# Performance work log

Measured on AMD Instinct MI355X. Metric: run time of the kernel, lower is better.

The kernel has to match this reference:

```python
import jax, jax.numpy as jnp
import numpy as np

B, N, D = 4, 4096, 512
E, H, TOPK = 4, 2048, 1
V_MAX, FEAT_CLAMP = 3.0, 10.0


def setup_inputs() -> dict:
    key = jax.random.key(0)
    ks = jax.random.split(key, 8)
    g = lambda k, shape, s: (jax.random.normal(k, shape, jnp.float32) * s)
    return {
        "x": g(ks[0], (B, N, D), 1.0),
        "gate_w": g(ks[1], (D, E), 0.02), "gate_b": jnp.zeros((E,), jnp.float32),
        "w1": g(ks[2], (E, D, H), 0.02), "b1": jnp.zeros((E, H), jnp.float32),
        "w2": g(ks[3], (E, H, D), 0.02), "b2": jnp.zeros((E, D), jnp.float32),
        "v_w": g(ks[4], (D,), 0.02), "v_b": jnp.zeros((), jnp.float32),
        "out_w": g(ks[5], (2, D), 0.02), "out_b": jnp.zeros((D,), jnp.float32),
        "bk_scale": jnp.asarray(1.0, jnp.float32),
    }


def _moe_ffn(x, gate_w, gate_b, w1, b1, w2, b2):
    # Sparse MoE FFN (eval mode, no dropout): top-k routing, softmax over top-k logits.
    logits = x @ gate_w + gate_b                       # (B,N,E)
    vals, idx = jax.lax.top_k(logits, TOPK)            # (B,N,K)
    wts = jax.nn.softmax(vals, axis=-1)                # (B,N,K); == 1.0 for top_k=1
    wfull = jnp.sum(jax.nn.one_hot(idx, E, dtype=x.dtype) * wts[..., None], axis=-2)  # (B,N,E)
    h = jax.nn.gelu(jnp.einsum('bnd,edh->benh', x, w1) + b1[None, :, None, :])
    y = jnp.einsum('benh,ehd->bend', h, w2) + b2[None, :, None, :]
    return jnp.einsum('bne,bend->bnd', wfull, y)


def _tridiag_green_diag(diag, sup, sub, z):
    # Diagonal of G = (T - z I)^{-1} for tridiagonal T via stable continuant ratios:
    #   L_i = theta_i/theta_{i-1},  R_i = phi_i/phi_{i+1},  G_ii = 1/(L_i + R_i - d_i)
    d = diag.astype(jnp.complex64) - z                 # (B,N)
    s = (sub * sup).astype(jnp.complex64)              # (B,N-1)
    dT = jnp.swapaxes(d, 0, 1)                         # (N,B)
    sT = jnp.swapaxes(s, 0, 1)                         # (N-1,B)

    def step(carry, inp):
        di, si = inp
        nxt = di - si / carry
        return nxt, nxt

    _, Lrest = jax.lax.scan(step, dT[0], (dT[1:], sT))
    L = jnp.concatenate([dT[:1], Lrest], axis=0)       # (N,B)
    _, Rrest = jax.lax.scan(step, dT[-1], (dT[:-1][::-1], sT[::-1]))
    R = jnp.concatenate([dT[-1:], Rrest], axis=0)[::-1]
    G = 1.0 / (L + R - dT)                             # (N,B)
    return jnp.swapaxes(G, 0, 1)                       # (B,N)


def reference(x, gate_w, gate_b, w1, b1, w2, b2, v_w, v_b, out_w, out_b, bk_scale):
    ffn_out = _moe_ffn(x, gate_w, gate_b, w1, b1, w2, b2)        # (B,N,D)
    v = jnp.clip(ffn_out @ v_w + v_b, -V_MAX, V_MAX)             # (B,N)
    he_diag = v - 2.0                                            # h0_diag_base = -2
    ones_off = jnp.ones((x.shape[0], x.shape[1] - 1), x.dtype)   # h0 sub/super = 1
    G = _tridiag_green_diag(he_diag, ones_off, ones_off, jnp.complex64(1j))
    feats = jnp.clip(jnp.stack([G.real, G.imag], axis=-1), -FEAT_CLAMP, FEAT_CLAMP)  # (B,N,2)
    spec = feats @ out_w + out_b                                 # (B,N,D)
    return ffn_out + bk_scale * spec
```

## Files before the change

kernel.cpp:

```cpp
#include <hip/hip_runtime.h>
#include <hip/hip_bf16.h>
#include <stdint.h>

#define TOK 16384
#define NSEQ 4096
#define BATCH 4
#define Dm 512
#define Em 4
#define Hm 2048

typedef __attribute__((ext_vector_type(4))) float f32x4;
typedef __attribute__((ext_vector_type(4))) unsigned int u32x4;

__device__ __forceinline__ unsigned short f2bf(float f) {
    union { float f; uint32_t u; } v; v.f = f;
    uint32_t u = v.u;
    uint32_t r = (u + 0x7FFFu + ((u >> 16) & 1u)) >> 16;
    return (unsigned short)r;
}

struct cpx { float re, im; };
__device__ __forceinline__ cpx cmul(cpx a, cpx b) { return { a.re*b.re - a.im*b.im, a.re*b.im + a.im*b.re }; }
__device__ __forceinline__ cpx csub(cpx a, cpx b) { return { a.re - b.re, a.im - b.im }; }
__device__ __forceinline__ cpx cadd(cpx a, cpx b) { return { a.re + b.re, a.im + b.im }; }
__device__ __forceinline__ cpx cdiv(cpx a, cpx b) {
    float inv = 1.0f / (b.re*b.re + b.im*b.im);
    return { (a.re*b.re + a.im*b.im)*inv, (a.im*b.re - a.re*b.im)*inv };
}

__device__ __forceinline__ void mfma_bf16(f32x4& acc, u32x4 a, u32x4 b) {
    asm("v_mfma_f32_16x16x32_bf16 %0, %1, %2, %0" : "+v"(acc) : "v"(a), "v"(b));
}

#define GLOAD_LDS16(g, l) \
    __builtin_amdgcn_global_load_lds((const __attribute__((address_space(1))) unsigned int*)(g), \
                                     (__attribute__((address_space(3))) unsigned int*)(l), 16, 0, 0)

__global__ __launch_bounds__(256) void gate_kernel(
    const float* __restrict__ x, const float* __restrict__ gate_w, const float* __restrict__ gate_b,
    unsigned short* __restrict__ xbf, int* __restrict__ expert_id)
{
    int wid = threadIdx.x >> 6, lane = threadIdx.x & 63;
    int t0 = (blockIdx.x * 4 + wid) * 8;

    const float4* gw4 = (const float4*)gate_w;
    float4 g[8];
#pragma unroll
    for (int j = 0; j < 8; j++) g[j] = gw4[lane * 8 + j];
    double gb0 = (double)gate_b[0], gb1 = (double)gate_b[1];
    double gb2 = (double)gate_b[2], gb3 = (double)gate_b[3];

    for (int tt = 0; tt < 8; tt++) {
        int t = t0 + tt;
        const float4* x4 = (const float4*)(x + (size_t)t * Dm);
        float4 xa = x4[lane * 2], xb = x4[lane * 2 + 1];

        uint4 pk;
        pk.x = (uint32_t)f2bf(xa.x) | ((uint32_t)f2bf(xa.y) << 16);
        pk.y = (uint32_t)f2bf(xa.z) | ((uint32_t)f2bf(xa.w) << 16);
        pk.z = (uint32_t)f2bf(xb.x) | ((uint32_t)f2bf(xb.y) << 16);
        pk.w = (uint32_t)f2bf(xb.z) | ((uint32_t)f2bf(xb.w) << 16);
        *(uint4*)(xbf + (size_t)t * Dm + lane * 8) = pk;

        float xv[8] = { xa.x, xa.y, xa.z, xa.w, xb.x, xb.y, xb.z, xb.w };
        double s0 = 0, s1 = 0, s2 = 0, s3 = 0;
#pragma unroll
        for (int j = 0; j < 8; j++) {
            s0 += (double)xv[j] * (double)g[j].x;
            s1 += (double)xv[j] * (double)g[j].y;
            s2 += (double)xv[j] * (double)g[j].z;
            s3 += (double)xv[j] * (double)g[j].w;
        }
#pragma unroll
        for (int off = 1; off < 64; off <<= 1) {
            s0 += __shfl_xor(s0, off);
            s1 += __shfl_xor(s1, off);
            s2 += __shfl_xor(s2, off);
            s3 += __shfl_xor(s3, off);
        }
        if (lane == 0) {
            double l0 = s0 + gb0, l1 = s1 + gb1, l2 = s2 + gb2, l3 = s3 + gb3;
            int e = 0; double best = l0;
            if (l1 > best) { best = l1; e = 1; }
            if (l2 > best) { best = l2; e = 2; }
            if (l3 > best) { best = l3; e = 3; }
            expert_id[t] = e;
        }
    }
}

__global__ __launch_bounds__(256) void transpose_cvt(
    const float* __restrict__ w1, const float* __restrict__ w2,
    unsigned short* __restrict__ w1t, unsigned short* __restrict__ w2t)
{
    int z = blockIdx.z;
    const float* src; unsigned short* dst; int R, C;
    if (z < 4) { src = w1 + (size_t)z * Dm * Hm; dst = w1t + (size_t)z * Hm * Dm; R = Dm; C = Hm; }
    else       { src = w2 + (size_t)(z - 4) * Hm * Dm; dst = w2t + (size_t)(z - 4) * Dm * Hm; R = Hm; C = Dm; }
    int c0 = blockIdx.x * 32, r0 = blockIdx.y * 32;
    if (c0 >= C || r0 >= R) return;
    __shared__ float tile[32][33];
    int tx = threadIdx.x & 31, ty = threadIdx.x >> 5;
#pragma unroll
    for (int i = 0; i < 4; i++)
        tile[ty + i * 8][tx] = src[(size_t)(r0 + ty + i * 8) * C + c0 + tx];
    __syncthreads();
#pragma unroll
    for (int i = 0; i < 4; i++)
        dst[(size_t)(c0 + ty + i * 8) * R + r0 + tx] = f2bf(tile[tx][ty + i * 8]);
}

__global__ __launch_bounds__(1024) void route_kernel(
    const int* __restrict__ expert_id, int* __restrict__ counts,
    int* __restrict__ offsets, int* __restrict__ rowmap)
{
    __shared__ int wcnt[16][4];
    __shared__ int woff[16][4];
    int wid = threadIdx.x >> 6, lane = threadIdx.x & 63;
    int base = wid * 1024;

    int myeid[16], myrank[16];
    int run0 = 0, run1 = 0, run2 = 0, run3 = 0;
#pragma unroll
    for (int s = 0; s < 16; s++) {
        int e = expert_id[base + s * 64 + lane];
        myeid[s] = e;
        unsigned long long b0 = __ballot(e & 1);
        unsigned long long b1 = __ballot(e & 2);
        unsigned long long m0 = (e & 1) ? b0 : ~b0;
        unsigned long long m1 = (e & 2) ? b1 : ~b1;
        unsigned long long same = m0 & m1;
        unsigned long long below = same & ((1ull << lane) - 1ull);
        int runh = (e == 0) ? run0 : (e == 1) ? run1 : (e == 2) ? run2 : run3;
        myrank[s] = runh + (int)__popcll(below);
        run0 += (int)__popcll(~b0 & ~b1);
        run1 += (int)__popcll(b0 & ~b1);
        run2 += (int)__popcll(~b0 & b1);
        run3 += (int)__popcll(b0 & b1);
    }
    if (lane == 0) {
        wcnt[wid][0] = run0; wcnt[wid][1] = run1; wcnt[wid][2] = run2; wcnt[wid][3] = run3;
    }
    __syncthreads();
    if (threadIdx.x == 0) {
        int t0 = 0, t1 = 0, t2 = 0, t3 = 0;
        for (int w = 0; w < 16; w++) {
            woff[w][0] = t0; woff[w][1] = t1; woff[w][2] = t2; woff[w][3] = t3;
            t0 += wcnt[w][0]; t1 += wcnt[w][1]; t2 += wcnt[w][2]; t3 += wcnt[w][3];
        }
        counts[0] = t0; counts[1] = t1; counts[2] = t2; counts[3] = t3;
        int o0 = 0, o1 = t0, o2 = t0 + t1, o3 = t0 + t1 + t2;
        offsets[0] = o0; offsets[1] = o1; offsets[2] = o2; offsets[3] = o3;
        for (int w = 0; w < 16; w++) {
            woff[w][0] += o0; woff[w][1] += o1; woff[w][2] += o2; woff[w][3] += o3;
        }
    }
    __syncthreads();
#pragma unroll
    for (int s = 0; s < 16; s++) {
        int e = myeid[s];
        rowmap[woff[wid][e] + myrank[s]] = base + s * 64 + lane;
    }
}

template<int KTOT, int NTOT, bool GATHER_A, bool GELU_EPI>
__global__ __launch_bounds__(256) void gemm_kernel(
    const unsigned short* __restrict__ A, const unsigned short* __restrict__ B,
    const float* __restrict__ bias,
    const int* __restrict__ counts, const int* __restrict__ offsets,
    const int* __restrict__ rowmap,
    unsigned short* __restrict__ Hout, float* __restrict__ Cout)
{
    int e = blockIdx.z;
    int Me = counts[e];
    int mblk = blockIdx.y;
    if (mblk * 128 >= Me) return;
    int base = offsets[e];
    int nblk = blockIdx.x;
    int t = threadIdx.x, wid = t >> 6, lane = t & 63;

    __shared__ __align__(16) unsigned short As[128 * 64];
    __shared__ __align__(16) unsigned short Bs[128 * 64];

    const unsigned short* agp[4];
    const unsigned short* bgp[4];
#pragma unroll
    for (int c = 0; c < 4; c++) {
        int f = c * 256 + t;
        int r = f >> 3;
        int kb = (f & 7) ^ (r & 7);
        int mr = mblk * 128 + r; if (mr >= Me) mr = Me - 1;
        int arow = GATHER_A ? rowmap[base + mr] : (base + mr);
        agp[c] = A + (size_t)arow * KTOT + kb * 8;
        int nr = nblk * 128 + r;
        bgp[c] = B + ((size_t)e * NTOT + nr) * (size_t)KTOT + kb * 8;
    }

    f32x4 acc[4][4] = {};
    int wm = wid >> 1, wn = wid & 1;

    for (int kt = 0; kt < KTOT / 64; kt++) {
        __syncthreads();
#pragma unroll
        for (int c = 0; c < 4; c++) {
            GLOAD_LDS16(agp[c] + kt * 64, As + (size_t)(c * 256 + wid * 64) * 8);
            GLOAD_LDS16(bgp[c] + kt * 64, Bs + (size_t)(c * 256 + wid * 64) * 8);
        }
        __syncthreads();
#pragma unroll
        for (int ks = 0; ks < 2; ks++) {
            u32x4 av[4], bv[4];
#pragma unroll
            for (int m = 0; m < 4; m++) {
                int ra = wm * 64 + m * 16 + (lane & 15);
                int g = (ks * 4 + (lane >> 4)) ^ (ra & 7);
                av[m] = *(const u32x4*)((const char*)As + ra * 128 + g * 16);
            }
#pragma unroll
            for (int n = 0; n < 4; n++) {
                int rb = wn * 64 + n * 16 + (lane & 15);
                int g = (ks * 4 + (lane >> 4)) ^ (rb & 7);
                bv[n] = *(const u32x4*)((const char*)Bs + rb * 128 + g * 16);
            }
#pragma unroll
            for (int m = 0; m < 4; m++)
#pragma unroll
                for (int n = 0; n < 4; n++)
                    mfma_bf16(acc[m][n], av[m], bv[n]);
        }
    }

#pragma unroll
    for (int n = 0; n < 4; n++) {
        int col = nblk * 128 + wn * 64 + n * 16 + (lane & 15);
        float bv = bias[e * NTOT + col];
#pragma unroll
        for (int m = 0; m < 4; m++) {
            int rbase = wm * 64 + m * 16 + ((lane >> 4) << 2);
#pragma unroll
            for (int j = 0; j < 4; j++) {
                int row = mblk * 128 + rbase + j;
                if (row < Me) {
                    float v = acc[m][n][j] + bv;
                    if (GELU_EPI) {
                        float u = 0.7978845608f * (v + 0.044715f * v * v * v);
                        float ex = __expf(2.0f * u);
                        float th = 1.0f - 2.0f / (ex + 1.0f);
                        float hv = 0.5f * v * (1.0f + th);
                        Hout[(size_t)(base + row) * NTOT + col] = f2bf(hv);
                    } else {
                        int tok = rowmap[base + row];
                        Cout[(size_t)tok * Dm + col] = v;
                    }
                }
            }
        }
    }
}

__global__ __launch_bounds__(256) void vdot_kernel(
    const float* __restrict__ out, const float* __restrict__ v_w, const float* __restrict__ v_b,
    float* __restrict__ dre)
{
    int wid = threadIdx.x >> 6, lane = threadIdx.x & 63;
    int t = blockIdx.x * 4 + wid;
    const float4* o4 = (const float4*)(out + (size_t)t * Dm);
    const float4* w4 = (const float4*)v_w;
    float4 a = o4[lane * 2], b = o4[lane * 2 + 1];
    float4 wa = w4[lane * 2], wb = w4[lane * 2 + 1];
    float s = a.x*wa.x + a.y*wa.y + a.z*wa.z + a.w*wa.w
            + b.x*wb.x + b.y*wb.y + b.z*wb.z + b.w*wb.w;
#pragma unroll
    for (int off = 1; off < 64; off <<= 1) s += __shfl_xor(s, off);
    if (lane == 0) {
        float v = s + v_b[0];
        v = fminf(fmaxf(v, -3.0f), 3.0f);
        dre[t] = v - 2.0f;
    }
}

#define SDI(i) ((i) + ((i) >> 6))
__global__ __launch_bounds__(64) void scan_kernel(
    const float* __restrict__ dre, float2* __restrict__ Lf, float2* __restrict__ Rb)
{
    int b = blockIdx.x >> 1, dir = blockIdx.x & 1;
    int lane = threadIdx.x;
    __shared__ float sd[4096 + 64];
    const float* src = dre + b * NSEQ;
    for (int i = lane; i < NSEQ; i += 64)
        sd[SDI(i)] = src[dir ? (NSEQ - 1 - i) : i];
    __syncthreads();

    cpx m00 = {1, 0}, m01 = {0, 0}, m10 = {0, 0}, m11 = {1, 0};
    int s0i = lane * 64;
#pragma unroll 4
    for (int j = 0; j < 64; j++) {
        cpx d = { sd[SDI(s0i + j)], -1.0f };
        cpx n00 = csub(cmul(d, m00), m10);
        cpx n01 = csub(cmul(d, m01), m11);
        m10 = m00; m11 = m01; m00 = n00; m01 = n01;
        if ((j & 15) == 15) {
            float mx = fmaxf(fmaxf(fmaxf(fabsf(m00.re), fabsf(m00.im)), fmaxf(fabsf(m01.re), fabsf(m01.im))),
                             fmaxf(fmaxf(fabsf(m10.re), fabsf(m10.im)), fmaxf(fabsf(m11.re), fabsf(m11.im))));
            float r = 1.0f / mx;
            m00.re *= r; m00.im *= r; m01.re *= r; m01.im *= r;
            m10.re *= r; m10.im *= r; m11.re *= r; m11.im *= r;
        }
    }

#pragma unroll
    for (int off = 1; off < 64; off <<= 1) {
        cpx q00, q01, q10, q11;
        q00.re = __shfl_up(m00.re, off); q00.im = __shfl_up(m00.im, off);
        q01.re = __shfl_up(m01.re, off); q01.im = __shfl_up(m01.im, off);
        q10.re = __shfl_up(m10.re, off); q10.im = __shfl_up(m10.im, off);
        q11.re = __shfl_up(m11.re, off); q11.im = __shfl_up(m11.im, off);
        if (lane >= off) {
            cpx r00 = cadd(cmul(m00, q00), cmul(m01, q10));
            cpx r01 = cadd(cmul(m00, q01), cmul(m01, q11));
            cpx r10 = cadd(cmul(m10, q00), cmul(m11, q10));
            cpx r11 = cadd(cmul(m10, q01), cmul(m11, q11));
            m00 = r00; m01 = r01; m10 = r10; m11 = r11;
            float mx = fmaxf(fmaxf(fmaxf(fabsf(m00.re), fabsf(m00.im)), fmaxf(fabsf(m01.re), fabsf(m01.im))),
                             fmaxf(fmaxf(fabsf(m10.re), fabsf(m10.im)), fmaxf(fabsf(m11.re), fabsf(m11.im))));
            float r = 1.0f / mx;
            m00.re *= r; m00.im *= r; m01.re *= r; m01.im *= r;
            m10.re *= r; m10.im *= r; m11.re *= r; m11.im *= r;
        }
    }

    cpx e00, e10;
    e00.re = __shfl_up(m00.re, 1); e00.im = __shfl_up(m00.im, 1);
    e10.re = __shfl_up(m10.re, 1); e10.im = __shfl_up(m10.im, 1);
    if (lane == 0) { e00 = {1, 0}; e10 = {0, 0}; }

    float2* outp = dir ? Rb : Lf;
    cpx Linv = cdiv(e10, e00);
#pragma unroll 4
    for (int j = 0; j < 64; j++) {
        int p = s0i + j;
        cpx d = { sd[SDI(p)], -1.0f };
        cpx L = csub(d, Linv);
        int idx = dir ? (NSEQ - 1 - p) : p;
        outp[b * NSEQ + idx] = make_float2(L.re, L.im);
        float inv = 1.0f / (L.re * L.re + L.im * L.im);
        Linv.re = L.re * inv; Linv.im = -L.im * inv;
    }
}

__global__ __launch_bounds__(256) void final_kernel(
    float* __restrict__ out, const float* __restrict__ dre,
    const float2* __restrict__ Lf, const float2* __restrict__ Rb,
    const float* __restrict__ out_w, const float* __restrict__ out_b,
    const float* __restrict__ bk)
{
    int t = blockIdx.x * 2 + (threadIdx.x >> 7);
    int c = threadIdx.x & 127;
    float2 L = Lf[t], R = Rb[t];
    float dr = dre[t];
    float denr = L.x + R.x - dr;
    float deni = L.y + R.y + 1.0f;
    float inv = 1.0f / (denr * denr + deni * deni);
    float f0 = fminf(fmaxf(denr * inv, -10.0f), 10.0f);
    float f1 = fminf(fmaxf(-deni * inv, -10.0f), 10.0f);
    float bks = bk[0];
    const float4* ow0 = (const float4*)out_w;
    const float4* ow1 = (const float4*)(out_w + Dm);
    const float4* ob4 = (const float4*)out_b;
    float4* o4 = (float4*)(out + (size_t)t * Dm);
    float4 w0 = ow0[c], w1v = ow1[c], ob = ob4[c];
    float4 y = o4[c];
    y.x += bks * (f0 * w0.x + f1 * w1v.x + ob.x);
    y.y += bks * (f0 * w0.y + f1 * w1v.y + ob.y);
    y.z += bks * (f0 * w0.z + f1 * w1v.z + ob.z);
    y.w += bks * (f0 * w0.w + f1 * w1v.w + ob.w);
    o4[c] = y;
}

constexpr size_t OFF_XBF    = 0;
constexpr size_t OFF_W1T    = 16777216;
constexpr size_t OFF_W2T    = OFF_W1T + 8388608;
constexpr size_t OFF_H      = OFF_W2T + 8388608;
constexpr size_t OFF_ROWMAP = OFF_H + 67108864;
constexpr size_t OFF_EID    = OFF_ROWMAP + 65536;
constexpr size_t OFF_DRE    = OFF_EID + 65536;
constexpr size_t OFF_LF     = OFF_DRE + 65536;
constexpr size_t OFF_RB     = OFF_LF + 131072;
constexpr size_t OFF_CNT    = OFF_RB + 131072;

extern "C" void kernel_launch(void* const* d_in, const int* in_sizes, int n_in,
                              void* d_out, int out_size, void* d_ws, size_t ws_size,
                              hipStream_t stream)
{
    const float* x      = (const float*)d_in[0];
    const float* gate_w = (const float*)d_in[1];
    const float* gate_b = (const float*)d_in[2];
    const float* w1     = (const float*)d_in[3];
    const float* b1     = (const float*)d_in[4];
    const float* w2     = (const float*)d_in[5];
    const float* b2     = (const float*)d_in[6];
    const float* v_w    = (const float*)d_in[7];
    const float* v_b    = (const float*)d_in[8];
    const float* out_w  = (const float*)d_in[9];
    const float* out_b  = (const float*)d_in[10];
    const float* bk     = (const float*)d_in[11];
    float* out = (float*)d_out;
    char* ws = (char*)d_ws;

    unsigned short* xbf = (unsigned short*)(ws + OFF_XBF);
    unsigned short* w1t = (unsigned short*)(ws + OFF_W1T);
    unsigned short* w2t = (unsigned short*)(ws + OFF_W2T);
    unsigned short* hbf = (unsigned short*)(ws + OFF_H);
    int* rowmap  = (int*)(ws + OFF_ROWMAP);
    int* eid     = (int*)(ws + OFF_EID);
    float* dre   = (float*)(ws + OFF_DRE);
    float2* Lf   = (float2*)(ws + OFF_LF);
    float2* Rb   = (float2*)(ws + OFF_RB);
    int* counts  = (int*)(ws + OFF_CNT);
    int* offsets = counts + 4;

    (void)in_sizes; (void)n_in; (void)out_size; (void)ws_size;

    gate_kernel<<<TOK / 32, 256, 0, stream>>>(x, gate_w, gate_b, xbf, eid);
    transpose_cvt<<<dim3(64, 64, 8), 256, 0, stream>>>(w1, w2, w1t, w2t);
    route_kernel<<<1, 1024, 0, stream>>>(eid, counts, offsets, rowmap);

    gemm_kernel<512, 2048, true, true><<<dim3(16, 128, 4), 256, 0, stream>>>(
        xbf, w1t, b1, counts, offsets, rowmap, hbf, nullptr);
    gemm_kernel<2048, 512, false, false><<<dim3(4, 128, 4), 256, 0, stream>>>(
        hbf, w2t, b2, counts, offsets, rowmap, nullptr, out);

    vdot_kernel<<<TOK / 4, 256, 0, stream>>>(out, v_w, v_b, dre);
    scan_kernel<<<8, 64, 0, stream>>>(dre, Lf, Rb);
    final_kernel<<<TOK / 2, 256, 0, stream>>>(out, dre, Lf, Rb, out_w, out_b, bk);
}
```

Measured before the change: 221.8 us.

## Double-buffer LDS tiles in MoE GEMM to overlap global loads with MFMA

The expert GEMM kernel now uses two LDS buffers for its A and B tiles. The next k-tile is loaded with direct-to-LDS global loads while MFMAs run on the current tile, and the per-iteration barrier count drops from two to one. LDS offsets for the swizzled fragment reads are also precomputed once, with the k-half selected by XOR. This doubles LDS use to 64KB per block, which may cut occupancy. The single barrier relies on the async loads having completed before the next iteration reads the buffer.

```diff
diff --git a/kernel.cpp b/kernel.cpp
--- a/kernel.cpp
+++ b/kernel.cpp
@@ -171,6 +171,7 @@
     const int* __restrict__ rowmap,
     unsigned short* __restrict__ Hout, float* __restrict__ Cout)
 {
+    constexpr int NT = KTOT / 64;
     int e = blockIdx.z;
     int Me = counts[e];
     int mblk = blockIdx.y;
@@ -179,8 +180,8 @@
     int nblk = blockIdx.x;
     int t = threadIdx.x, wid = t >> 6, lane = t & 63;
 
-    __shared__ __align__(16) unsigned short As[128 * 64];
-    __shared__ __align__(16) unsigned short Bs[128 * 64];
+    __shared__ __align__(16) unsigned short As[2][128 * 64];
+    __shared__ __align__(16) unsigned short Bs[2][128 * 64];
 
     const unsigned short* agp[4];
     const unsigned short* bgp[4];
@@ -196,39 +197,60 @@
         bgp[c] = B + ((size_t)e * NTOT + nr) * (size_t)KTOT + kb * 8;
     }
 
+    int wm = wid >> 1, wn = wid & 1;
+    int hi = lane >> 4;
+
+    int aoffs[4], boffs[4];
+#pragma unroll
+    for (int m = 0; m < 4; m++) {
+        int ra = wm * 64 + m * 16 + (lane & 15);
+        aoffs[m] = ra * 128 + ((hi ^ (ra & 7)) << 4);
+    }
+#pragma unroll
+    for (int n = 0; n < 4; n++) {
+        int rb = wn * 64 + n * 16 + (lane & 15);
+        boffs[n] = rb * 128 + ((hi ^ (rb & 7)) << 4);
+    }
+
     f32x4 acc[4][4] = {};
-    int wm = wid >> 1, wn = wid & 1;
-
-    for (int kt = 0; kt < KTOT / 64; kt++) {
-        __syncthreads();
-#pragma unroll
-        for (int c = 0; c < 4; c++) {
-            GLOAD_LDS16(agp[c] + kt * 64, As + (size_t)(c * 256 + wid * 64) * 8);
-            GLOAD_LDS16(bgp[c] + kt * 64, Bs + (size_t)(c * 256 + wid * 64) * 8);
-        }
-        __syncthreads();
+
+#define STAGE_T(bufi, kt) do { \
+    unsigned short* asd = &As[bufi][0]; \
+    unsigned short* bsd = &Bs[bufi][0]; \
+    _Pragma("unroll") \
+    for (int c = 0; c < 4; c++) { \
+        GLOAD_LDS16(agp[c] + (kt) * 64, asd + (c * 256 + wid * 64) * 8); \
+        GLOAD_LDS16(bgp[c] + (kt) * 64, bsd + (c * 256 + wid * 64) * 8); \
+    } \
+} while (0)
+
+    STAGE_T(0, 0);
+    __syncthreads();
+
+    int cur = 0;
+    for (int kt = 0; kt < NT; ++kt) {
+        if (kt + 1 < NT) STAGE_T(cur ^ 1, kt + 1);
+
+        const char* ab = (const char*)&As[cur][0];
+        const char* bb = (const char*)&Bs[cur][0];
 #pragma unroll
         for (int ks = 0; ks < 2; ks++) {
+            int kx = ks << 6;
             u32x4 av[4], bv[4];
 #pragma unroll
-            for (int m = 0; m < 4; m++) {
-                int ra = wm * 64 + m * 16 + (lane & 15);
-                int g = (ks * 4 + (lane >> 4)) ^ (ra & 7);
-                av[m] = *(const u32x4*)((const char*)As + ra * 128 + g * 16);
-            }
-#pragma unroll
-            for (int n = 0; n < 4; n++) {
-                int rb = wn * 64 + n * 16 + (lane & 15);
-                int g = (ks * 4 + (lane >> 4)) ^ (rb & 7);
-                bv[n] = *(const u32x4*)((const char*)Bs + rb * 128 + g * 16);
-            }
+            for (int m = 0; m < 4; m++) av[m] = *(const u32x4*)(ab + (aoffs[m] ^ kx));
+#pragma unroll
+            for (int n = 0; n < 4; n++) bv[n] = *(const u32x4*)(bb + (boffs[n] ^ kx));
 #pragma unroll
             for (int m = 0; m < 4; m++)
 #pragma unroll
                 for (int n = 0; n < 4; n++)
                     mfma_bf16(acc[m][n], av[m], bv[n]);
         }
-    }
+        __syncthreads();
+        cur ^= 1;
+    }
+#undef STAGE_T
 
 #pragma unroll
     for (int n = 0; n < 4; n++) {
```

After: 256.8 us. 15.8% more time.
